# Kernel tuning notes

Measured on AMD Instinct MI355X. Metric: run time of the kernel, lower is better.

## Reference

```python
import jax, jax.numpy as jnp
import numpy as np

BS, NE, F = 128, 512, 6
HEADS, DPH = 4, 4
N_EMBD = HEADS * DPH  # 16


def setup_inputs() -> dict:
    key = jax.random.key(0)
    k_inp, k_mask, kq, kk, kv, kp = jax.random.split(key, 6)
    inp = jax.random.normal(k_inp, (BS, NE, F), dtype=jnp.float32)
    # binary float mask; guarantee at least one unmasked entity per batch row
    mask = (jax.random.uniform(k_mask, (BS, NE)) < 0.8).astype(jnp.float32)
    mask = mask.at[:, 0].set(1.0)
    std = 1.0 / np.sqrt(N_EMBD)
    Wq = jax.random.normal(kq, (N_EMBD, F), dtype=jnp.float32) * std
    Wk = jax.random.normal(kk, (N_EMBD, F), dtype=jnp.float32) * std
    Wv = jax.random.normal(kv, (N_EMBD, F), dtype=jnp.float32) * std
    Wpost = jax.random.normal(kp, (F, N_EMBD), dtype=jnp.float32) * std
    return {"inp": inp, "mask": mask, "Wq": Wq, "Wk": Wk, "Wv": Wv, "Wpost": Wpost}


def reference(inp, mask, Wq, Wk, Wv, Wpost):
    bs, ne, f = inp.shape
    x_in = inp * mask[:, :, None]                       # mask input entities
    # projections (Linear with weight [out,in]): x @ W.T
    q = (x_in @ Wq.T).reshape(bs, ne, HEADS, DPH)
    k = (x_in @ Wk.T).reshape(bs, ne, HEADS, DPH)
    v = (x_in @ Wv.T).reshape(bs, ne, HEADS, DPH)
    scale = 1.0 / np.sqrt(N_EMBD / HEADS)               # 1/sqrt(4)
    logits = jnp.einsum('bqhd,bkhd->bhqk', q, k) * scale  # [bs,H,NE,NE]
    logits = logits + 1e9 * (mask[:, None, None, :] - 1.0)  # mask keys pre-softmax
    p = jax.nn.softmax(logits, axis=-1)
    p = p * mask[:, None, :, None]                      # zero masked query rows
    att = jnp.einsum('bhqk,bkhd->bqhd', p, v).reshape(bs, ne, N_EMBD)
    x = x_in + att @ Wpost.T                            # residual
    # mask-corrected mean/std normalization over dims [1,2]
    N = jnp.sum(mask, axis=1)[:, None, None]            # [bs,1,1] valid entity count
    mu = jnp.mean(x, axis=(1, 2), keepdims=True) * (ne / N)
    x2 = x + (1.0 - mask[:, :, None]) * mu              # fill masked slots with mu
    m2 = jnp.mean(x2, axis=(1, 2), keepdims=True)
    var = jnp.sum((x2 - m2) ** 2, axis=(1, 2), keepdims=True) / (ne * f - 1)  # unbiased
    std = jnp.sqrt(var) * jnp.sqrt((f * ne - 1.0) / (f * N - 1.0))
    xn = (x - mu) / (std + 1e-6)
    # masked mean pool over entities
    summed = jnp.sum(xn * mask[:, :, None], axis=1)     # [bs,F]
    denom = jnp.sum(mask, axis=1)[:, None]
    return summed / denom
```

## Files before the change

kernel.cpp:

```cpp
#include <hip/hip_runtime.h>
#include <math.h>

#define BS    128
#define NE    512
#define F     6
#define NH    4
#define DPH   4
#define NEMBD 16

#define CPAD 129

__global__ __launch_bounds__(512) void attn_kernel(
    const float* __restrict__ inp, const float* __restrict__ mask,
    const float* __restrict__ Wq, const float* __restrict__ Wk,
    const float* __restrict__ Wv, float* __restrict__ att_out)
{
    const int blk = blockIdx.x;
    const int b = blk >> 2;
    const int h = blk & 3;
    const int t = threadIdx.x;
    const int c = t & 3;
    const int g = t >> 2;

    __shared__ float4 sk[4 * CPAD];
    __shared__ float4 sv[4 * CPAD];
    __shared__ float  sn[8];

    {
        const int e = t;
        const float me = mask[b * NE + e];
        const float2* rp = (const float2*)(inp + ((size_t)(b * NE + e)) * F);
        const float2 r0 = rp[0], r1 = rp[1], r2 = rp[2];
        const float x0 = r0.x * me, x1 = r0.y * me, x2 = r1.x * me,
                    x3 = r1.y * me, x4 = r2.x * me, x5 = r2.y * me;
        const float* wk = Wk + h * DPH * F;
        const float* wv = Wv + h * DPH * F;
        float kk[DPH], vv[DPH];
        #pragma unroll
        for (int d = 0; d < DPH; ++d) {
            const float* w = wk + d * F;
            kk[d] = x0*w[0] + x1*w[1] + x2*w[2] + x3*w[3] + x4*w[4] + x5*w[5];
            w = wv + d * F;
            vv[d] = x0*w[0] + x1*w[1] + x2*w[2] + x3*w[3] + x4*w[4] + x5*w[5];
        }
        const int ce = e >> 7, je = e & 127;
        sk[ce * CPAD + je] = make_float4(kk[0], kk[1], kk[2], kk[3]);
        sv[ce * CPAD + je] = make_float4(vv[0], vv[1], vv[2], vv[3]);

        float mw = me;
        #pragma unroll
        for (int off = 32; off >= 1; off >>= 1) mw += __shfl_down(mw, off);
        if ((t & 63) == 0) sn[t >> 6] = mw;
    }

    float q[4][DPH];
    {
        const float* wq = Wq + h * DPH * F;
        #pragma unroll
        for (int r = 0; r < 4; ++r) {
            const int row = 4 * g + r;
            const float mr = mask[b * NE + row];
            const float2* rp = (const float2*)(inp + ((size_t)(b * NE + row)) * F);
            const float2 r0 = rp[0], r1 = rp[1], r2 = rp[2];
            const float x0 = r0.x * mr, x1 = r0.y * mr, x2 = r1.x * mr,
                        x3 = r1.y * mr, x4 = r2.x * mr, x5 = r2.y * mr;
            #pragma unroll
            for (int d = 0; d < DPH; ++d) {
                const float* w = wq + d * F;
                q[r][d] = 0.5f * (x0*w[0] + x1*w[1] + x2*w[2] + x3*w[3] + x4*w[4] + x5*w[5]);
            }
        }
    }

    __syncthreads();

    float Nb = 0.f;
    #pragma unroll
    for (int w = 0; w < 8; ++w) Nb += sn[w];
    const float lcorr = 512.0f - Nb;

    const float4* kbase = sk + c * CPAD;
    const float4* vbase = sv + c * CPAD;
    float l[4] = {0.f, 0.f, 0.f, 0.f};
    float a[4][DPH];
    #pragma unroll
    for (int r = 0; r < 4; ++r)
        #pragma unroll
        for (int d = 0; d < DPH; ++d) a[r][d] = 0.f;

    #pragma unroll 4
    for (int jj = 0; jj < 128; ++jj) {
        const float4 kv = kbase[jj];
        const float4 uv = vbase[jj];
        #pragma unroll
        for (int r = 0; r < 4; ++r) {
            const float s = fmaf(q[r][0], kv.x, fmaf(q[r][1], kv.y,
                             fmaf(q[r][2], kv.z, q[r][3] * kv.w)));
            const float e = __expf(s);
            l[r] += e;
            a[r][0] = fmaf(e, uv.x, a[r][0]);
            a[r][1] = fmaf(e, uv.y, a[r][1]);
            a[r][2] = fmaf(e, uv.z, a[r][2]);
            a[r][3] = fmaf(e, uv.w, a[r][3]);
        }
    }

    #pragma unroll
    for (int m = 1; m <= 2; m <<= 1) {
        #pragma unroll
        for (int r = 0; r < 4; ++r) {
            l[r] += __shfl_xor(l[r], m);
            #pragma unroll
            for (int d = 0; d < DPH; ++d) a[r][d] += __shfl_xor(a[r][d], m);
        }
    }

    const int row = 4 * g + c;
    const float mi = mask[b * NE + row];
    const float lr = l[c] - lcorr;
    const float rscale = mi / lr;
    float4* o = (float4*)(att_out + ((size_t)(b * NE + row)) * NEMBD + h * DPH);
    *o = make_float4(a[c][0] * rscale, a[c][1] * rscale,
                     a[c][2] * rscale, a[c][3] * rscale);
}

__global__ __launch_bounds__(NE) void epi_kernel(
    const float* __restrict__ inp, const float* __restrict__ mask,
    const float* __restrict__ Wpost, const float* __restrict__ att,
    float* __restrict__ out)
{
    const int b = blockIdx.x;
    const int i = threadIdx.x;
    const int wave = i >> 6;
    const int lane = i & 63;

    __shared__ float swp[F * NEMBD];
    __shared__ float red[64];

    if (i < F * NEMBD) swp[i] = Wpost[i];
    __syncthreads();

    const float mi = mask[b * NE + i];
    const float* row = inp + ((size_t)(b * NE + i)) * F;
    const float* ar  = att + ((size_t)(b * NE + i)) * NEMBD;

    float a[NEMBD];
    #pragma unroll
    for (int t = 0; t < NEMBD; t += 4) {
        const float4 v = *(const float4*)(ar + t);
        a[t] = v.x; a[t+1] = v.y; a[t+2] = v.z; a[t+3] = v.w;
    }

    float x[F];
    #pragma unroll
    for (int f = 0; f < F; ++f) {
        float acc = row[f] * mi;
        #pragma unroll
        for (int t = 0; t < NEMBD; ++t) acc = fmaf(a[t], swp[f * NEMBD + t], acc);
        x[f] = acc;
    }

    float rs = x[0] + x[1] + x[2] + x[3] + x[4] + x[5];
    float rn = mi;
    #pragma unroll
    for (int off = 32; off >= 1; off >>= 1) {
        rs += __shfl_down(rs, off);
        rn += __shfl_down(rn, off);
    }
    if (lane == 0) { red[wave * 2] = rs; red[wave * 2 + 1] = rn; }
    __syncthreads();
    float S = 0.f, N = 0.f;
    #pragma unroll
    for (int w = 0; w < 8; ++w) { S += red[w * 2]; N += red[w * 2 + 1]; }

    const float mu     = S / (6.0f * N);
    const float sum_x2 = S + (NE - N) * 6.0f * mu;
    const float m2     = sum_x2 / (NE * 6.0f);
    const float add    = (1.0f - mi) * mu;

    float ss = 0.f;
    #pragma unroll
    for (int f = 0; f < F; ++f) { const float d = x[f] + add - m2; ss = fmaf(d, d, ss); }

    __syncthreads();
    #pragma unroll
    for (int off = 32; off >= 1; off >>= 1) ss += __shfl_down(ss, off);
    if (lane == 0) red[wave] = ss;
    __syncthreads();
    float vs = 0.f;
    #pragma unroll
    for (int w = 0; w < 8; ++w) vs += red[w];

    const float var  = vs / (NE * 6.0f - 1.0f);
    const float stdv = sqrtf(var) * sqrtf((6.0f * NE - 1.0f) / (6.0f * N - 1.0f));
    const float inv  = 1.0f / (stdv + 1e-6f);

    float y[F];
    #pragma unroll
    for (int f = 0; f < F; ++f) y[f] = mi * (x[f] - mu) * inv;

    __syncthreads();
    #pragma unroll
    for (int off = 32; off >= 1; off >>= 1) {
        #pragma unroll
        for (int f = 0; f < F; ++f) y[f] += __shfl_down(y[f], off);
    }
    if (lane == 0) {
        #pragma unroll
        for (int f = 0; f < F; ++f) red[wave * F + f] = y[f];
    }
    __syncthreads();
    if (i < F) {
        float t = 0.f;
        #pragma unroll
        for (int w = 0; w < 8; ++w) t += red[w * F + i];
        out[b * F + i] = t / N;
    }
}

extern "C" void kernel_launch(void* const* d_in, const int* in_sizes, int n_in,
                              void* d_out, int out_size, void* d_ws, size_t ws_size,
                              hipStream_t stream) {
    const float* inp   = (const float*)d_in[0];
    const float* mask  = (const float*)d_in[1];
    const float* Wq    = (const float*)d_in[2];
    const float* Wk    = (const float*)d_in[3];
    const float* Wv    = (const float*)d_in[4];
    const float* Wpost = (const float*)d_in[5];
    float* out = (float*)d_out;
    float* att = (float*)d_ws;

    attn_kernel<<<BS * NH, NE, 0, stream>>>(inp, mask, Wq, Wk, Wv, att);
    epi_kernel<<<BS, NE, 0, stream>>>(inp, mask, Wpost, att, out);
}
```

Baseline: 108.8 us.

## Fuse output projection into attention via atomics, split query rows, use exp2

Splits each (batch, head) block into two query halves of 256 threads, with 8 query rows per thread over 8 key chunks. The output projection Wpost is folded into the attention kernel, which atomically adds each head's contribution into a padded residual buffer. A new init kernel fills that buffer with the masked input beforehand. The epilogue now reads only 8 floats per entity, and the softmax uses exp2 with log2e folded into the query scale. This aims to cut the 16-float attention intermediate traffic and raise block count and occupancy. In exchange it adds a third launch, atomic contention from four heads per row, and recomputes K/V in both halves.

```diff
diff --git a/kernel.cpp b/kernel.cpp
--- a/kernel.cpp
+++ b/kernel.cpp
@@ -7,28 +7,55 @@
 #define NH    4
 #define DPH   4
 #define NEMBD 16
-
-#define CPAD 129
-
-__global__ __launch_bounds__(512) void attn_kernel(
+#define XPAD  8
+
+#if __has_builtin(__builtin_amdgcn_exp2f)
+#define EXP2(x) __builtin_amdgcn_exp2f(x)
+#else
+#define EXP2(x) exp2f(x)
+#endif
+
+__global__ __launch_bounds__(256) void init_x(
+    const float* __restrict__ inp, const float* __restrict__ mask,
+    float* __restrict__ x)
+{
+    const int e = blockIdx.x * 256 + threadIdx.x;
+    const float me = mask[e];
+    const float2* rp = (const float2*)(inp + (size_t)e * F);
+    const float2 r0 = rp[0], r1 = rp[1], r2 = rp[2];
+    float4* o = (float4*)(x + (size_t)e * XPAD);
+    o[0] = make_float4(r0.x * me, r0.y * me, r1.x * me, r1.y * me);
+    o[1] = make_float4(r2.x * me, r2.y * me, 0.f, 0.f);
+}
+
+#define CH    8
+#define CKEYS 64
+#define CPAD  65
+
+__global__ __launch_bounds__(256) void attn_kernel(
     const float* __restrict__ inp, const float* __restrict__ mask,
     const float* __restrict__ Wq, const float* __restrict__ Wk,
-    const float* __restrict__ Wv, float* __restrict__ att_out)
+    const float* __restrict__ Wv, const float* __restrict__ Wpost,
+    float* __restrict__ x)
 {
-    const int blk = blockIdx.x;
-    const int b = blk >> 2;
-    const int h = blk & 3;
-    const int t = threadIdx.x;
-    const int c = t & 3;
-    const int g = t >> 2;
-
-    __shared__ float4 sk[4 * CPAD];
-    __shared__ float4 sv[4 * CPAD];
-    __shared__ float  sn[8];
-
-    {
-        const int e = t;
+    const int blk  = blockIdx.x;
+    const int b    = blk >> 3;
+    const int h    = (blk >> 1) & 3;
+    const int half = blk & 1;
+    const int t    = threadIdx.x;
+    const int c    = t & 7;
+    const int g    = t >> 3;
+
+    __shared__ float4 sk[CH * CPAD];
+    __shared__ float4 sv[CH * CPAD];
+    __shared__ float  sn[4];
+
+    float mw = 0.f;
+    #pragma unroll
+    for (int s = 0; s < 2; ++s) {
+        const int e = t + s * 256;
         const float me = mask[b * NE + e];
+        mw += me;
         const float2* rp = (const float2*)(inp + ((size_t)(b * NE + e)) * F);
         const float2 r0 = rp[0], r1 = rp[1], r2 = rp[2];
         const float x0 = r0.x * me, x1 = r0.y * me, x2 = r1.x * me,
@@ -43,22 +70,20 @@
             w = wv + d * F;
             vv[d] = x0*w[0] + x1*w[1] + x2*w[2] + x3*w[3] + x4*w[4] + x5*w[5];
         }
-        const int ce = e >> 7, je = e & 127;
-        sk[ce * CPAD + je] = make_float4(kk[0], kk[1], kk[2], kk[3]);
-        sv[ce * CPAD + je] = make_float4(vv[0], vv[1], vv[2], vv[3]);
-
-        float mw = me;
-        #pragma unroll
-        for (int off = 32; off >= 1; off >>= 1) mw += __shfl_down(mw, off);
-        if ((t & 63) == 0) sn[t >> 6] = mw;
-    }
-
-    float q[4][DPH];
+        sk[(e >> 6) * CPAD + (e & 63)] = make_float4(kk[0], kk[1], kk[2], kk[3]);
+        sv[(e >> 6) * CPAD + (e & 63)] = make_float4(vv[0], vv[1], vv[2], vv[3]);
+    }
+    #pragma unroll
+    for (int off = 32; off >= 1; off >>= 1) mw += __shfl_down(mw, off);
+    if ((t & 63) == 0) sn[t >> 6] = mw;
+
+    const float QS = 0.5f * 1.44269504088896340736f;
+    float q[8][DPH];
     {
         const float* wq = Wq + h * DPH * F;
         #pragma unroll
-        for (int r = 0; r < 4; ++r) {
-            const int row = 4 * g + r;
+        for (int r = 0; r < 8; ++r) {
+            const int row = half * 256 + 8 * g + r;
             const float mr = mask[b * NE + row];
             const float2* rp = (const float2*)(inp + ((size_t)(b * NE + row)) * F);
             const float2 r0 = rp[0], r1 = rp[1], r2 = rp[2];
@@ -67,36 +92,36 @@
             #pragma unroll
             for (int d = 0; d < DPH; ++d) {
                 const float* w = wq + d * F;
-                q[r][d] = 0.5f * (x0*w[0] + x1*w[1] + x2*w[2] + x3*w[3] + x4*w[4] + x5*w[5]);
+                q[r][d] = QS * (x0*w[0] + x1*w[1] + x2*w[2] + x3*w[3] + x4*w[4] + x5*w[5]);
             }
         }
     }
 
     __syncthreads();
 
-    float Nb = 0.f;
-    #pragma unroll
-    for (int w = 0; w < 8; ++w) Nb += sn[w];
+    const float Nb = sn[0] + sn[1] + sn[2] + sn[3];
     const float lcorr = 512.0f - Nb;
 
-    const float4* kbase = sk + c * CPAD;
-    const float4* vbase = sv + c * CPAD;
-    float l[4] = {0.f, 0.f, 0.f, 0.f};
-    float a[4][DPH];
-    #pragma unroll
-    for (int r = 0; r < 4; ++r)
+    const float4* kb = sk + c * CPAD;
+    const float4* vb = sv + c * CPAD;
+    float l[8];
+    float a[8][DPH];
+    #pragma unroll
+    for (int r = 0; r < 8; ++r) {
+        l[r] = 0.f;
         #pragma unroll
         for (int d = 0; d < DPH; ++d) a[r][d] = 0.f;
-
-    #pragma unroll 4
-    for (int jj = 0; jj < 128; ++jj) {
-        const float4 kv = kbase[jj];
-        const float4 uv = vbase[jj];
-        #pragma unroll
-        for (int r = 0; r < 4; ++r) {
+    }
+
+    #pragma unroll 2
+    for (int j = 0; j < CKEYS; ++j) {
+        const float4 kv = kb[j];
+        const float4 uv = vb[j];
+        #pragma unroll
+        for (int r = 0; r < 8; ++r) {
             const float s = fmaf(q[r][0], kv.x, fmaf(q[r][1], kv.y,
                              fmaf(q[r][2], kv.z, q[r][3] * kv.w)));
-            const float e = __expf(s);
+            const float e = EXP2(s);
             l[r] += e;
             a[r][0] = fmaf(e, uv.x, a[r][0]);
             a[r][1] = fmaf(e, uv.y, a[r][1]);
@@ -106,27 +131,38 @@
     }
 
     #pragma unroll
-    for (int m = 1; m <= 2; m <<= 1) {
-        #pragma unroll
-        for (int r = 0; r < 4; ++r) {
+    for (int m = 1; m <= 4; m <<= 1) {
+        #pragma unroll
+        for (int r = 0; r < 8; ++r) {
             l[r] += __shfl_xor(l[r], m);
             #pragma unroll
             for (int d = 0; d < DPH; ++d) a[r][d] += __shfl_xor(a[r][d], m);
         }
     }
 
-    const int row = 4 * g + c;
+    float lsel = l[0], p0 = a[0][0], p1 = a[0][1], p2 = a[0][2], p3 = a[0][3];
+    #pragma unroll
+    for (int r = 1; r < 8; ++r) {
+        if (r == c) { lsel = l[r]; p0 = a[r][0]; p1 = a[r][1]; p2 = a[r][2]; p3 = a[r][3]; }
+    }
+
+    const int row = half * 256 + 8 * g + c;
     const float mi = mask[b * NE + row];
-    const float lr = l[c] - lcorr;
-    const float rscale = mi / lr;
-    float4* o = (float4*)(att_out + ((size_t)(b * NE + row)) * NEMBD + h * DPH);
-    *o = make_float4(a[c][0] * rscale, a[c][1] * rscale,
-                     a[c][2] * rscale, a[c][3] * rscale);
+    const float lr = lsel - lcorr;
+    const float rs = mi / lr;
+    p0 *= rs; p1 *= rs; p2 *= rs; p3 *= rs;
+
+    float* xr = x + ((size_t)(b * NE + row)) * XPAD;
+    #pragma unroll
+    for (int f = 0; f < F; ++f) {
+        const float* w = Wpost + f * NEMBD + h * DPH;
+        const float cf = fmaf(p0, w[0], fmaf(p1, w[1], fmaf(p2, w[2], p3 * w[3])));
+        atomicAdd(xr + f, cf);
+    }
 }
 
 __global__ __launch_bounds__(NE) void epi_kernel(
-    const float* __restrict__ inp, const float* __restrict__ mask,
-    const float* __restrict__ Wpost, const float* __restrict__ att,
+    const float* __restrict__ mask, const float* __restrict__ x,
     float* __restrict__ out)
 {
     const int b = blockIdx.x;
@@ -134,40 +170,21 @@
     const int wave = i >> 6;
     const int lane = i & 63;
 
-    __shared__ float swp[F * NEMBD];
     __shared__ float red[64];
 
-    if (i < F * NEMBD) swp[i] = Wpost[i];
-    __syncthreads();
-
     const float mi = mask[b * NE + i];
-    const float* row = inp + ((size_t)(b * NE + i)) * F;
-    const float* ar  = att + ((size_t)(b * NE + i)) * NEMBD;
-
-    float a[NEMBD];
-    #pragma unroll
-    for (int t = 0; t < NEMBD; t += 4) {
-        const float4 v = *(const float4*)(ar + t);
-        a[t] = v.x; a[t+1] = v.y; a[t+2] = v.z; a[t+3] = v.w;
-    }
-
-    float x[F];
-    #pragma unroll
-    for (int f = 0; f < F; ++f) {
-        float acc = row[f] * mi;
-        #pragma unroll
-        for (int t = 0; t < NEMBD; ++t) acc = fmaf(a[t], swp[f * NEMBD + t], acc);
-        x[f] = acc;
-    }
-
-    float rs = x[0] + x[1] + x[2] + x[3] + x[4] + x[5];
+    const float4* xr = (const float4*)(x + ((size_t)(b * NE + i)) * XPAD);
+    const float4 v0 = xr[0], v1 = xr[1];
+    const float xv[F] = {v0.x, v0.y, v0.z, v0.w, v1.x, v1.y};
+
+    float rsum = xv[0] + xv[1] + xv[2] + xv[3] + xv[4] + xv[5];
     float rn = mi;
     #pragma unroll
     for (int off = 32; off >= 1; off >>= 1) {
-        rs += __shfl_down(rs, off);
-        rn += __shfl_down(rn, off);
-    }
-    if (lane == 0) { red[wave * 2] = rs; red[wave * 2 + 1] = rn; }
+        rsum += __shfl_down(rsum, off);
+        rn   += __shfl_down(rn, off);
+    }
+    if (lane == 0) { red[wave * 2] = rsum; red[wave * 2 + 1] = rn; }
     __syncthreads();
     float S = 0.f, N = 0.f;
     #pragma unroll
@@ -180,7 +197,7 @@
 
     float ss = 0.f;
     #pragma unroll
-    for (int f = 0; f < F; ++f) { const float d = x[f] + add - m2; ss = fmaf(d, d, ss); }
+    for (int f = 0; f < F; ++f) { const float d = xv[f] + add - m2; ss = fmaf(d, d, ss); }
 
     __syncthreads();
     #pragma unroll
@@ -197,7 +214,7 @@
 
     float y[F];
     #pragma unroll
-    for (int f = 0; f < F; ++f) y[f] = mi * (x[f] - mu) * inv;
+    for (int f = 0; f < F; ++f) y[f] = mi * (xv[f] - mu) * inv;
 
     __syncthreads();
     #pragma unroll
@@ -211,10 +228,10 @@
     }
     __syncthreads();
     if (i < F) {
-        float t = 0.f;
-        #pragma unroll
-        for (int w = 0; w < 8; ++w) t += red[w * F + i];
-        out[b * F + i] = t / N;
+        float tt = 0.f;
+        #pragma unroll
+        for (int w = 0; w < 8; ++w) tt += red[w * F + i];
+        out[b * F + i] = tt / N;
     }
 }
 
@@ -228,8 +245,9 @@
     const float* Wv    = (const float*)d_in[4];
     const float* Wpost = (const float*)d_in[5];
     float* out = (float*)d_out;
-    float* att = (float*)d_ws;
-
-    attn_kernel<<<BS * NH, NE, 0, stream>>>(inp, mask, Wq, Wk, Wv, att);
-    epi_kernel<<<BS, NE, 0, stream>>>(inp, mask, Wpost, att, out);
-}
+    float* x   = (float*)d_ws;
+
+    init_x    <<<BS * NE / 256, 256, 0, stream>>>(inp, mask, x);
+    attn_kernel<<<BS * NH * 2, 256, 0, stream>>>(inp, mask, Wq, Wk, Wv, Wpost, x);
+    epi_kernel <<<BS, NE, 0, stream>>>(mask, x, out);
+}
```

After: 121.3 us. +11.5%, slower.
